# Performance work log

Measured on AMD Instinct MI355X. Metric: run time of the kernel, lower is better.

Reference implementation:

```python
import jax, jax.numpy as jnp
from jax import lax
import numpy as np

BLOCK = 256
EPS = 1e-6


def rms_norm(x, w):
    var = jnp.mean(jnp.square(x), axis=-1, keepdims=True)
    return x * lax.rsqrt(var + EPS) * w


def lightning_attn(q, k, v, slope):
    # q,k,v: [b,h,n,d]; slope: [h] positive decay rates
    b, h, n, d = q.shape
    nb = n // BLOCK
    ar = jnp.arange(1, BLOCK + 1, dtype=q.dtype)          # [BLOCK]
    s = slope[:, None, None]                               # [h,1,1]
    q_decay = jnp.exp(-s * ar[:, None])                    # [h,BLOCK,1]
    k_decay = jnp.exp(-s * (BLOCK - ar)[:, None])          # [h,BLOCK,1]
    idx = ar[:, None] - ar[None, :]                        # [BLOCK,BLOCK]
    diag_decay = jnp.exp(jnp.where(idx >= 0, -s * idx, -jnp.inf))  # [h,B,B]
    block_decay = jnp.exp(-slope * BLOCK)[None, :, None, None]     # [1,h,1,1]

    def to_blocks(x):
        return jnp.moveaxis(x.reshape(b, h, nb, BLOCK, d), 2, 0)   # [nb,b,h,B,d]

    qb, kb, vb = to_blocks(q), to_blocks(k), to_blocks(v)

    def step(kv, blk):
        qi, ki, vi = blk                                   # [b,h,B,d]
        inter = jnp.einsum('bhmd,bhde->bhme', qi * q_decay, kv)
        qk = jnp.einsum('bhmd,bhkd->bhmk', qi, ki) * diag_decay
        intra = jnp.einsum('bhmk,bhke->bhme', qk, vi)
        kv_new = block_decay * kv + jnp.einsum('bhmd,bhme->bhde', ki * k_decay, vi)
        return kv_new, inter + intra

    kv0 = jnp.zeros((b, h, d, d), q.dtype)
    kv, out = lax.scan(step, kv0, (qb, kb, vb))            # out: [nb,b,h,B,d]
    out = jnp.moveaxis(out, 0, 2).reshape(b, h, n, d)
    return out, kv


def setup_inputs() -> dict:
    key = jax.random.key(0)
    ks = jax.random.split(key, 6)
    b, n, hidden, h, dh = 2, 4096, 2048, 16, 128
    return {
        'hidden_states': jax.random.normal(ks[0], (b, n, hidden), jnp.float32),
        'slope_rate': jax.random.uniform(ks[1], (h,), jnp.float32, 1e-3, 0.2),
        'w_qkv': jax.random.normal(ks[2], (3 * h * dh, hidden), jnp.float32) * 0.02,
        'w_gate': jax.random.normal(ks[3], (h * dh, hidden), jnp.float32) * 0.02,
        'w_out': jax.random.normal(ks[4], (hidden, h * dh), jnp.float32) * 0.02,
        'norm_w': jnp.ones((h * dh,), jnp.float32),
    }


def reference(hidden_states, slope_rate, w_qkv, w_gate, w_out, norm_w):
    b, n, hidden = hidden_states.shape
    h = slope_rate.shape[0]
    dh = hidden // h
    qkv = jax.nn.silu(hidden_states @ w_qkv.T)             # [b,n,3*h*dh]
    qkv = qkv.reshape(b, n, 3, h, dh)
    q = jnp.transpose(qkv[:, :, 0], (0, 2, 1, 3))          # [b,h,n,dh]
    k = jnp.transpose(qkv[:, :, 1], (0, 2, 1, 3))
    v = jnp.transpose(qkv[:, :, 2], (0, 2, 1, 3))
    attn_out, _kv = lightning_attn(q, k, v, slope_rate)
    attn_out = jnp.transpose(attn_out, (0, 2, 1, 3)).reshape(b, n, h * dh)
    out = rms_norm(attn_out, norm_w)
    gate = jax.nn.sigmoid(hidden_states @ w_gate.T)
    out = (gate * out) @ w_out.T
    return out
```

## Files before the change

### kernel.cpp

```cpp
#include <hip/hip_runtime.h>


typedef unsigned short u16;
typedef __bf16 bf16x8 __attribute__((ext_vector_type(8)));
typedef float f32x4 __attribute__((ext_vector_type(4)));

#define SEQ 4096
#define HID 2048

__device__ __forceinline__ u16 f2bf(float f) {
    union { float f; unsigned u; } v; v.f = f;
    unsigned r = v.u + 0x7fffu + ((v.u >> 16) & 1u);
    return (u16)(r >> 16);
}
__device__ __forceinline__ float bf2f(u16 u) {
    union { unsigned u; float f; } v; v.u = ((unsigned)u) << 16; return v.f;
}

typedef __attribute__((address_space(1))) unsigned char gas_u8;
typedef __attribute__((address_space(3))) unsigned char las_u8;
__device__ __forceinline__ void gld16(const void* g, void* l) {
    __builtin_amdgcn_global_load_lds((gas_u8*)g, (las_u8*)l, 16, 0, 0);
}

__global__ __launch_bounds__(256) void castk(const float* __restrict__ in,
                                             u16* __restrict__ out) {
    const size_t i = (size_t)blockIdx.x * 256 + threadIdx.x;
    const float4 f = *(const float4*)&in[i * 4];
    uint2 o;
    o.x = (unsigned)f2bf(f.x) | ((unsigned)f2bf(f.y) << 16);
    o.y = (unsigned)f2bf(f.z) | ((unsigned)f2bf(f.w) << 16);
    *(uint2*)&out[i * 4] = o;
}

template <int MODE>
__global__ __launch_bounds__(512, 2) void gemm256(const u16* __restrict__ A,
                                                  const u16* __restrict__ Bm,
                                                  void* __restrict__ Cv,
                                                  void* __restrict__ aux,
                                                  void* __restrict__ aux2) {
    constexpr int NTN = (MODE == 0) ? 32 : 8;
    constexpr int NT  = 32;
    extern __shared__ u16 smem[];

    const int bid = blockIdx.x;
    const int xcd = bid & 7, l = bid >> 3;
    int tm, tn;
    if constexpr (MODE == 0) {
        tm = xcd * 4 + (l & 3);
        tn = ((l >> 2) & 7) | ((l >> 5) << 3);
    } else {
        const int wgid = xcd * 32 + l;
        tm = wgid / NTN; tn = wgid % NTN;
    }

    const int tid  = threadIdx.x;
    const int lane = tid & 63, wv = tid >> 6;
    const int quad = lane >> 4, cl = lane & 15;
    const int wm = (wv & 1) * 128, wn = (wv >> 1) * 64;

    const int srw  = tid >> 3;
    const int colo = ((tid & 7) ^ (srw & 7)) * 8;
    const u16* gA0 = A  + (size_t)(tm * 256 + srw) * HID + colo;
    const u16* gB0 = Bm + (size_t)(tn * 256 + srw) * HID + colo;

    const int x0 = ((quad       ^ (cl & 7)) * 8);
    const int x1 = (((4 + quad) ^ (cl & 7)) * 8);

    f32x4 acc[8][4];
    const f32x4 zero = {0.f, 0.f, 0.f, 0.f};
    #pragma unroll
    for (int a = 0; a < 8; a++)
        #pragma unroll
        for (int b = 0; b < 4; b++) acc[a][b] = zero;

    bf16x8 af[8], b0[4], b1[4];

    auto STG = [&](int kt, int mat, int hh) {
        const u16* g = (mat ? gB0 : gA0) + (size_t)(hh * 128) * HID + kt * 64;
        u16* lp = smem + (kt & 1) * 32768 + mat * 16384 + hh * 8192 + wv * 512;
        gld16(g, lp);
        gld16(g + (size_t)64 * HID, lp + 4096);
    };
    auto LDA = [&](int qm, int ab) {
        #pragma unroll
        for (int mi = 0; mi < 4; mi++) {
            const int rr = (wm + qm * 64 + mi * 16 + cl) * 64 + ab;
            af[mi * 2 + 0] = *(const bf16x8*)&smem[rr + x0];
            af[mi * 2 + 1] = *(const bf16x8*)&smem[rr + x1];
        }
    };
    auto LDB = [&](bf16x8* d, int qn, int bb2) {
        #pragma unroll
        for (int ni = 0; ni < 2; ni++) {
            const int rr = (wn + qn * 32 + ni * 16 + cl) * 64 + bb2;
            d[ni * 2 + 0] = *(const bf16x8*)&smem[rr + x0];
            d[ni * 2 + 1] = *(const bf16x8*)&smem[rr + x1];
        }
    };
    auto MM = [&](int qm, int qn, const bf16x8* bv) {
        #pragma unroll
        for (int mi = 0; mi < 4; mi++)
            #pragma unroll
            for (int ni = 0; ni < 2; ni++) {
                f32x4 c = acc[qm * 4 + mi][qn * 2 + ni];
                c = __builtin_amdgcn_mfma_f32_16x16x32_bf16(af[mi * 2 + 0], bv[ni * 2 + 0], c, 0, 0, 0);
                c = __builtin_amdgcn_mfma_f32_16x16x32_bf16(af[mi * 2 + 1], bv[ni * 2 + 1], c, 0, 0, 0);
                acc[qm * 4 + mi][qn * 2 + ni] = c;
            }
    };

    STG(0, 1, 0); STG(0, 1, 1); STG(0, 0, 0); STG(0, 0, 1);
    STG(1, 1, 0); STG(1, 1, 1); STG(1, 0, 0);
    asm volatile("s_waitcnt vmcnt(6)" ::: "memory");
    __builtin_amdgcn_s_barrier();
    LDA(0, 0); LDB(b0, 0, 16384);

    #pragma unroll 2
    for (int t = 0; t < NT; ++t) {
        const int ab  = (t & 1) * 32768;
        const int bb2 = ab + 16384;
        const int nab = ((t + 1) & 1) * 32768;
        if (t + 1 < NT) STG(t + 1, 0, 1);
        __builtin_amdgcn_s_barrier();
        asm volatile("s_waitcnt lgkmcnt(0)" ::: "memory");
        __builtin_amdgcn_s_setprio(1); MM(0, 0, b0); __builtin_amdgcn_s_setprio(0);
        LDB(b1, 1, bb2);
        __builtin_amdgcn_s_barrier();
        if (t + 2 < NT) STG(t + 2, 1, 0);
        __builtin_amdgcn_s_barrier();
        asm volatile("s_waitcnt lgkmcnt(0)" ::: "memory");
        __builtin_amdgcn_s_setprio(1); MM(0, 1, b1); __builtin_amdgcn_s_setprio(0);
        LDA(1, ab);
        __builtin_amdgcn_s_barrier();
        if (t + 2 < NT) STG(t + 2, 1, 1);
        __builtin_amdgcn_s_barrier();
        asm volatile("s_waitcnt lgkmcnt(0)" ::: "memory");
        __builtin_amdgcn_s_setprio(1); MM(1, 1, b1); __builtin_amdgcn_s_setprio(0);
        __builtin_amdgcn_s_barrier();
        if (t + 2 < NT) {
            STG(t + 2, 0, 0);
            asm volatile("s_waitcnt vmcnt(6)" ::: "memory");
        } else {
            asm volatile("s_waitcnt vmcnt(0)" ::: "memory");
        }
        __builtin_amdgcn_s_barrier();
        __builtin_amdgcn_s_setprio(1); MM(1, 0, b0); __builtin_amdgcn_s_setprio(0);
        if (t + 1 < NT) { LDA(0, nab); LDB(b0, 0, nab + 16384); }
        __builtin_amdgcn_s_barrier();
    }

    if constexpr (MODE == 0) {
        const int grp = tn * 2 + (wn >> 7);
        const int which = grp >> 4, hd = grp & 15;
        const int n64 = wn & 64;
        if (which == 2) {
            const size_t bz = (size_t)((tm >> 4) * 256 + hd * 16 + (tm & 15));
            u16* tdst = (u16*)aux + bz * 32768;
            #pragma unroll
            for (int a = 0; a < 8; a++) {
                const int mm = wm + (a >> 2) * 64 + (a & 3) * 16 + quad * 4;
                #pragma unroll
                for (int b = 0; b < 4; b++) {
                    const int d = n64 + (b >> 1) * 32 + (b & 1) * 16 + cl;
                    u16 p[4];
                    #pragma unroll
                    for (int r = 0; r < 4; r++) {
                        const float x = acc[a][b][r];
                        p[r] = f2bf(x / (1.f + __expf(-x)));
                    }
                    uint2 pk;
                    pk.x = (unsigned)p[0] | ((unsigned)p[1] << 16);
                    pk.y = (unsigned)p[2] | ((unsigned)p[3] << 16);
                    *(uint2*)&tdst[(size_t)d * 256 + mm] = pk;
                }
            }
            return;
        }
        u16* dst = (which == 0) ? (u16*)Cv
                 : (which == 1) ? (u16*)Cv + (size_t)16777216
                                : (u16*)aux2;
        #pragma unroll
        for (int a = 0; a < 8; a++)
            #pragma unroll
            for (int b = 0; b < 4; b++)
                #pragma unroll
                for (int r = 0; r < 4; r++) {
                    const int m = tm * 256 + wm + (a >> 2) * 64 + (a & 3) * 16 + quad * 4 + r;
                    const int col = hd * 128 + n64 + (b >> 1) * 32 + (b & 1) * 16 + cl;
                    const float x = acc[a][b][r];
                    const float v = (which == 3) ? 1.f / (1.f + __expf(-x))
                                                 : x / (1.f + __expf(-x));
                    dst[(size_t)m * HID + col] = f2bf(v);
                }
        return;
    } else {
        float* C = (float*)Cv;
        #pragma unroll
        for (int a = 0; a < 8; a++)
            #pragma unroll
            for (int b = 0; b < 4; b++)
                #pragma unroll
                for (int r = 0; r < 4; r++) {
                    const int m = tm * 256 + wm + (a >> 2) * 64 + (a & 3) * 16 + quad * 4 + r;
                    const int n = tn * 256 + wn + (b >> 1) * 32 + (b & 1) * 16 + cl;
                    C[(size_t)m * HID + n] = acc[a][b][r];
                }
    }
}

#define M_KVT   4

template <int MODE>
__global__ __launch_bounds__(256) void gemm_nt(const u16* __restrict__ A,
                                               const u16* __restrict__ Bm,
                                               void* __restrict__ Cv,
                                               const float* __restrict__ slope,
                                               int bz0,
                                               void* __restrict__ aux,
                                               void* __restrict__ aux2) {
    const int tid = threadIdx.x;
    const int bz  = blockIdx.z + bz0;

    __shared__ u16 smem[8192];
    u16 (*As)[32] = (u16(*)[32])smem;
    u16 (*Bs)[32] = (u16(*)[32])(smem + 4096);

    const int lane = tid & 63, wv = tid >> 6;
    const int wm = (wv & 1) * 64, wn = (wv >> 1) * 64;
    const int quad = lane >> 4, cl = lane & 15;
    const int lr = lane >> 2;
    const int lc = (lane & 3) * 8;
    u16* lA = &As[wv * 32][0];
    u16* lB = &Bs[wv * 32][0];

    f32x4 acc[4][4];
    const f32x4 zero = {0.f, 0.f, 0.f, 0.f};
    #pragma unroll
    for (int mi = 0; mi < 4; mi++)
        #pragma unroll
        for (int ni = 0; ni < 4; ni++) acc[mi][ni] = zero;

    const u16* Ab = A + (size_t)bz * 32768;
    const u16* Bb = Bm + (size_t)bz * 32768;
    const u16* gA = Ab + (size_t)(wv * 32 + lr) * 256 + lc;
    const u16* gB = Bb + (size_t)(wv * 32 + lr) * 256 + lc;

    for (int k0 = 0; k0 < 256; k0 += 32) {
        __syncthreads();
        gld16(gA + k0,                  lA);
        gld16(gA + k0 + (size_t)16 * 256, lA + 16 * 32);
        gld16(gB + k0,                  lB);
        gld16(gB + k0 + (size_t)16 * 256, lB + 16 * 32);
        __syncthreads();
        const int ko = quad * 8;
        bf16x8 af[4], bfv[4];
        #pragma unroll
        for (int mi = 0; mi < 4; mi++) af[mi] = *(const bf16x8*)&As[wm + mi * 16 + cl][ko];
        #pragma unroll
        for (int ni = 0; ni < 4; ni++) bfv[ni] = *(const bf16x8*)&Bs[wn + ni * 16 + cl][ko];
        #pragma unroll
        for (int mi = 0; mi < 4; mi++)
            #pragma unroll
            for (int ni = 0; ni < 4; ni++)
                acc[mi][ni] = __builtin_amdgcn_mfma_f32_16x16x32_bf16(af[mi], bfv[ni], acc[mi][ni], 0, 0, 0);
    }

    #pragma unroll
    for (int mi = 0; mi < 4; mi++)
        #pragma unroll
        for (int ni = 0; ni < 4; ni++)
            #pragma unroll
            for (int r = 0; r < 4; r++) {
                const int m = wm + mi * 16 + quad * 4 + r;
                const int n = wn + ni * 16 + cl;
                ((float*)Cv)[(size_t)bz * 16384 + m * 128 + n] = acc[mi][ni][r];
            }
}

__global__ __launch_bounds__(256) void fused_pv(const u16* __restrict__ qb,
                                                const u16* __restrict__ kb,
                                                const u16* __restrict__ ST,
                                                const u16* __restrict__ vT,
                                                u16* __restrict__ attn,
                                                const float* __restrict__ slope) {
    __shared__ u16 smem[28672];
    u16* q_lds = smem;
    u16* k_lds = smem + 16384;
    u16* P_lds = smem + 20480;
    u16* Bs    = smem + 24576;

    const int tm = blockIdx.x;
    const int bz = blockIdx.z;
    const int bb = bz >> 8, hh = (bz >> 4) & 15, jb = bz & 15;
    const float s_ = slope[hh];

    const int tid  = threadIdx.x;
    const int lane = tid & 63, wv = tid >> 6;
    const int quad = lane >> 4, cl = lane & 15;
    const int wm = (wv & 1) * 64, wn = (wv >> 1) * 64;
    const int lr = lane >> 2, lc = (lane & 3) * 8;
    const int pcb = (wv >> 1) * 16;

    const size_t rowbase = (size_t)(bb * SEQ + jb * 256);

    const u16* gq = qb + (rowbase + tm * 128 + wv * 32 + lr) * HID + hh * 128 + lc;
    u16* lq = q_lds + wv * 1024 + lr * 32 + lc;
    #pragma unroll
    for (int ks = 0; ks < 4; ks++) {
        gld16(gq + ks * 32,                 lq + ks * 4096);
        gld16(gq + ks * 32 + 16 * HID,      lq + ks * 4096 + 512);
    }

    f32x4 acc[4][4];
    const f32x4 zero = {0.f, 0.f, 0.f, 0.f};
    #pragma unroll
    for (int mi = 0; mi < 4; mi++)
        #pragma unroll
        for (int ni = 0; ni < 4; ni++) acc[mi][ni] = zero;

    const u16* gS = ST + (size_t)bz * 16384 + (size_t)(wv * 32 + lr) * 128 + lc;
    u16* lB = Bs + wv * 1024 + lr * 32 + lc;
    #pragma unroll
    for (int ks = 0; ks < 4; ks++) {
        __syncthreads();
        gld16(gS + ks * 32,            lB);
        gld16(gS + ks * 32 + 16 * 128, lB + 512);
        __syncthreads();
        bf16x8 af[4], bfv[4];
        #pragma unroll
        for (int mi = 0; mi < 4; mi++)
            af[mi] = *(const bf16x8*)&q_lds[ks * 4096 + (wm + mi * 16 + cl) * 32 + quad * 8];
        #pragma unroll
        for (int ni = 0; ni < 4; ni++)
            bfv[ni] = *(const bf16x8*)&Bs[(wn + ni * 16 + cl) * 32 + quad * 8];
        #pragma unroll
        for (int mi = 0; mi < 4; mi++)
            #pragma unroll
            for (int ni = 0; ni < 4; ni++)
                acc[mi][ni] = __builtin_amdgcn_mfma_f32_16x16x32_bf16(af[mi], bfv[ni], acc[mi][ni], 0, 0, 0);
    }
    #pragma unroll
    for (int mi = 0; mi < 4; mi++)
        #pragma unroll
        for (int r = 0; r < 4; r++) {
            const int m = tm * 128 + wm + mi * 16 + quad * 4 + r;
            const float qd = __expf(-s_ * (float)(m + 1));
            #pragma unroll
            for (int ni = 0; ni < 4; ni++) acc[mi][ni][r] *= qd;
        }

    const int kmax = (tm == 0) ? 128 : 256;
    const u16* gV = vT + (size_t)bz * 32768 + (size_t)(wv * 32 + lr) * 256 + lc;
    const int krow = tid >> 4;
    const int kcol = (((tid & 15) ^ (krow & 7)) * 8);
    u16* lk = k_lds + wv * 512 + lane * 8;
    const int kvr = pcb + cl;

    for (int kv0 = 0; kv0 < kmax; kv0 += 32) {
        __syncthreads();
        gld16(kb + (rowbase + kv0 +      krow) * HID + hh * 128 + kcol, lk);
        gld16(kb + (rowbase + kv0 + 16 + krow) * HID + hh * 128 + kcol, lk + 2048);
        gld16(gV + kv0,            lB);
        gld16(gV + kv0 + 16 * 256, lB + 512);
        __syncthreads();
        f32x4 acc2[4];
        #pragma unroll
        for (int mi = 0; mi < 4; mi++) acc2[mi] = zero;
        #pragma unroll
        for (int ds = 0; ds < 4; ds++) {
            bf16x8 bk = *(const bf16x8*)&k_lds[kvr * 128 + (((ds * 4 + quad) ^ (kvr & 7)) * 8)];
            #pragma unroll
            for (int mi = 0; mi < 4; mi++) {
                bf16x8 aq = *(const bf16x8*)&q_lds[ds * 4096 + (wm + mi * 16 + cl) * 32 + quad * 8];
                acc2[mi] = __builtin_amdgcn_mfma_f32_16x16x32_bf16(aq, bk, acc2[mi], 0, 0, 0);
            }
        }
        #pragma unroll
        for (int mi = 0; mi < 4; mi++)
            #pragma unroll
            for (int r = 0; r < 4; r++) {
                const int row = wm + mi * 16 + quad * 4 + r;
                const int mb  = tm * 128 + row;
                const int kv  = kv0 + pcb + cl;
                const int d   = mb - kv;
                const float x = acc2[mi][r];
                P_lds[row * 32 + pcb + cl] = f2bf(d >= 0 ? x * __expf(-s_ * (float)d) : 0.f);
            }
        __syncthreads();
        bf16x8 afp[4], bfv[4];
        #pragma unroll
        for (int mi = 0; mi < 4; mi++)
            afp[mi] = *(const bf16x8*)&P_lds[(wm + mi * 16 + cl) * 32 + quad * 8];
        #pragma unroll
        for (int ni = 0; ni < 4; ni++)
            bfv[ni] = *(const bf16x8*)&Bs[(wn + ni * 16 + cl) * 32 + quad * 8];
        #pragma unroll
        for (int mi = 0; mi < 4; mi++)
            #pragma unroll
            for (int ni = 0; ni < 4; ni++)
                acc[mi][ni] = __builtin_amdgcn_mfma_f32_16x16x32_bf16(afp[mi], bfv[ni], acc[mi][ni], 0, 0, 0);
    }

    #pragma unroll
    for (int mi = 0; mi < 4; mi++)
        #pragma unroll
        for (int ni = 0; ni < 4; ni++)
            #pragma unroll
            for (int r = 0; r < 4; r++) {
                const int m = tm * 128 + wm + mi * 16 + quad * 4 + r;
                const int n = wn + ni * 16 + cl;
                attn[(rowbase + m) * HID + hh * 128 + n] = f2bf(acc[mi][ni][r]);
            }
}

__global__ __launch_bounds__(256) void transpose_k(const u16* __restrict__ kb,
                                                   u16* __restrict__ kTs,
                                                   const float* __restrict__ slope) {
    __shared__ u16 t[128][137];
    const int bz = blockIdx.x;
    const int bb = bz >> 8, hh = (bz >> 4) & 15, jb = bz & 15;
    const int tid = threadIdx.x;
    const float s_ = slope[hh];
    const u16* src = kb + ((size_t)(bb * SEQ + jb * 256)) * HID + hh * 128;
    u16* dst = kTs + (size_t)bz * 32768;

    for (int half = 0; half < 2; half++) {
        #pragma unroll
        for (int i = 0; i < 8; i++) {
            const int flat = tid + 256 * i;
            const int row = flat >> 4, c8 = (flat & 15) * 8;
            *(uint4*)&t[row][c8] = *(const uint4*)&src[(size_t)(half * 128 + row) * HID + c8];
        }
        __syncthreads();
        #pragma unroll
        for (int i = 0; i < 8; i++) {
            const int flat = tid + 256 * i;
            const int d = flat >> 4, mc = (flat & 15) * 8;
            u16 p[8];
            #pragma unroll
            for (int j = 0; j < 8; j++) {
                const int m = half * 128 + mc + j;
                p[j] = f2bf(bf2f(t[mc + j][d]) * __expf(-s_ * (float)(255 - m)));
            }
            uint4 pk;
            pk.x = (unsigned)p[0] | ((unsigned)p[1] << 16);
            pk.y = (unsigned)p[2] | ((unsigned)p[3] << 16);
            pk.z = (unsigned)p[4] | ((unsigned)p[5] << 16);
            pk.w = (unsigned)p[6] | ((unsigned)p[7] << 16);
            *(uint4*)&dst[(size_t)d * 256 + half * 128 + mc] = pk;
        }
        __syncthreads();
    }
}

__global__ __launch_bounds__(256) void scan_kv(const float* __restrict__ KVT,
                                               u16* __restrict__ ST,
                                               const float* __restrict__ slope) {
    const int bh = blockIdx.x >> 4, ch = blockIdx.x & 15;
    const int off = ch * 1024 + threadIdx.x * 4;
    const float bd = __expf(-256.f * slope[bh & 15]);
    float4 st = {0.f, 0.f, 0.f, 0.f};
    for (int j = 0; j < 16; j++) {
        const size_t base = ((size_t)(bh * 16 + j)) * 16384 + off;
        uint2 o;
        o.x = (unsigned)f2bf(st.x) | ((unsigned)f2bf(st.y) << 16);
        o.y = (unsigned)f2bf(st.z) | ((unsigned)f2bf(st.w) << 16);
        *(uint2*)&ST[base] = o;
        const float4 kv = *(const float4*)&KVT[base];
        st.x = bd * st.x + kv.x;
        st.y = bd * st.y + kv.y;
        st.z = bd * st.z + kv.z;
        st.w = bd * st.w + kv.w;
    }
}

__global__ __launch_bounds__(256) void rmsnorm_gate(const u16* __restrict__ attn,
                                                    const u16* __restrict__ gate,
                                                    const float* __restrict__ nw,
                                                    u16* __restrict__ y) {
    const int r = blockIdx.x, tid = threadIdx.x;
    const size_t base = (size_t)r * HID + tid * 8;
    const uint4 a = *(const uint4*)&attn[base];
    float x[8];
    x[0] = bf2f(a.x & 0xffff); x[1] = bf2f(a.x >> 16);
    x[2] = bf2f(a.y & 0xffff); x[3] = bf2f(a.y >> 16);
    x[4] = bf2f(a.z & 0xffff); x[5] = bf2f(a.z >> 16);
    x[6] = bf2f(a.w & 0xffff); x[7] = bf2f(a.w >> 16);
    float s = 0.f;
    #pragma unroll
    for (int i = 0; i < 8; i++) s += x[i] * x[i];
    #pragma unroll
    for (int off = 32; off > 0; off >>= 1) s += __shfl_down(s, off);
    __shared__ float red[4];
    if ((tid & 63) == 0) red[tid >> 6] = s;
    __syncthreads();
    const float tot = red[0] + red[1] + red[2] + red[3];
    const float sc = rsqrtf(tot * (1.f / 2048.f) + 1e-6f);
    const uint4 g = *(const uint4*)&gate[base];
    float gv[8];
    gv[0] = bf2f(g.x & 0xffff); gv[1] = bf2f(g.x >> 16);
    gv[2] = bf2f(g.y & 0xffff); gv[3] = bf2f(g.y >> 16);
    gv[4] = bf2f(g.z & 0xffff); gv[5] = bf2f(g.z >> 16);
    gv[6] = bf2f(g.w & 0xffff); gv[7] = bf2f(g.w >> 16);
    const float4 w0 = *(const float4*)&nw[tid * 8];
    const float4 w1 = *(const float4*)&nw[tid * 8 + 4];
    const float wv[8] = {w0.x, w0.y, w0.z, w0.w, w1.x, w1.y, w1.z, w1.w};
    u16 o[8];
    #pragma unroll
    for (int i = 0; i < 8; i++) o[i] = f2bf(gv[i] * x[i] * sc * wv[i]);
    uint4 ov;
    ov.x = (unsigned)o[0] | ((unsigned)o[1] << 16);
    ov.y = (unsigned)o[2] | ((unsigned)o[3] << 16);
    ov.z = (unsigned)o[4] | ((unsigned)o[5] << 16);
    ov.w = (unsigned)o[6] | ((unsigned)o[7] << 16);
    *(uint4*)&y[base] = ov;
}

extern "C" void kernel_launch(void* const* d_in, const int* in_sizes, int n_in,
                              void* d_out, int out_size, void* d_ws, size_t ws_size,
                              hipStream_t stream) {
    const float* hidden = (const float*)d_in[0];
    const float* slope  = (const float*)d_in[1];
    const float* w_qkv  = (const float*)d_in[2];
    const float* w_gate = (const float*)d_in[3];
    const float* w_out  = (const float*)d_in[4];
    const float* norm_w = (const float*)d_in[5];
    float* out = (float*)d_out;

    char* w = (char*)d_ws;
    u16* qb   = (u16*)(w);
    u16* kb   = (u16*)(w +  33554432);
    u16* kTs  = (u16*)(w +  67108864);
    u16* hid_bf = (u16*)(w + 100663296);
    u16* vT   = (u16*)(w + 134217728);
    u16* gate = (u16*)(w + 167772160);
    u16* wqkv_bf  = (u16*)(w + 201326592);
    u16* wgate_bf = (u16*)(w + 201326592 + 25165824);
    float* KVT  = (float*)hid_bf;
    u16*   ST   = kTs;
    u16*   wout_bf = kb;
    u16*   attn = wqkv_bf;
    u16*   y    = kTs;

    static bool s_attr = false;
    if (!s_attr) {
        (void)hipFuncSetAttribute((const void*)gemm256<0>,
                                  hipFuncAttributeMaxDynamicSharedMemorySize, 131072);
        (void)hipFuncSetAttribute((const void*)gemm256<1>,
                                  hipFuncAttributeMaxDynamicSharedMemorySize, 131072);
        s_attr = true;
    }

    castk<<<16384, 256, 0, stream>>>(hidden, hid_bf);
    castk<<<12288, 256, 0, stream>>>(w_qkv,  wqkv_bf);
    castk<<< 4096, 256, 0, stream>>>(w_gate, wgate_bf);

    gemm256<0><<<dim3(1024), dim3(512), 131072, stream>>>(hid_bf, wqkv_bf, qb, vT, gate);
    transpose_k     <<<512,             256, 0, stream>>>(kb, kTs, slope);
    gemm_nt<M_KVT ><<<dim3(1, 1, 512),  256, 0, stream>>>(vT, kTs, KVT, slope, 0, nullptr, nullptr);
    scan_kv         <<<512,             256, 0, stream>>>(KVT, ST, slope);
    fused_pv        <<<dim3(2, 1, 512), 256, 0, stream>>>(qb, kb, ST, vT, attn, slope);
    castk<<< 4096, 256, 0, stream>>>(w_out, wout_bf);
    rmsnorm_gate    <<<8192,            256, 0, stream>>>(attn, gate, norm_w, y);
    gemm256<1><<<dim3(256), dim3(512), 131072, stream>>>(y, wout_bf, (void*)out, nullptr, nullptr);
}
```

Before: 447.9 us.

## Fuse K transpose-decay into QKV GEMM epilogue and merge cast kernels

The QKV GEMM epilogue now writes the decayed, transposed K tile directly into the kTs buffer, so the separate transpose_k kernel and its re-read of K from global memory are gone. The three fp32-to-bf16 cast launches are merged into one kernel that picks its source by block range. In exchange the GEMM epilogue does extra exp work, and the transposed stores are 8-byte writes strided across rows, which may coalesce poorly and add register pressure to the epilogue.

```diff
diff --git a/kernel.cpp b/kernel.cpp
--- a/kernel.cpp
+++ b/kernel.cpp
@@ -33,12 +33,29 @@
     *(uint2*)&out[i * 4] = o;
 }
 
+__global__ __launch_bounds__(256) void castk3(const float* __restrict__ a, u16* __restrict__ ao,
+                                              const float* __restrict__ b, u16* __restrict__ bo,
+                                              const float* __restrict__ c, u16* __restrict__ co) {
+    const int bid = blockIdx.x;
+    const float* src; u16* dst; size_t i;
+    if (bid < 16384)      { src = a; dst = ao; i = (size_t)bid * 256 + threadIdx.x; }
+    else if (bid < 28672) { src = b; dst = bo; i = (size_t)(bid - 16384) * 256 + threadIdx.x; }
+    else                  { src = c; dst = co; i = (size_t)(bid - 28672) * 256 + threadIdx.x; }
+    const float4 f = *(const float4*)&src[i * 4];
+    uint2 o;
+    o.x = (unsigned)f2bf(f.x) | ((unsigned)f2bf(f.y) << 16);
+    o.y = (unsigned)f2bf(f.z) | ((unsigned)f2bf(f.w) << 16);
+    *(uint2*)&dst[i * 4] = o;
+}
+
 template <int MODE>
 __global__ __launch_bounds__(512, 2) void gemm256(const u16* __restrict__ A,
                                                   const u16* __restrict__ Bm,
                                                   void* __restrict__ Cv,
                                                   void* __restrict__ aux,
-                                                  void* __restrict__ aux2) {
+                                                  void* __restrict__ aux2,
+                                                  u16* __restrict__ kTs,
+                                                  const float* __restrict__ slope) {
     constexpr int NTN = (MODE == 0) ? 32 : 8;
     constexpr int NT  = 32;
     extern __shared__ u16 smem[];
@@ -193,6 +210,30 @@
                                                  : x / (1.f + __expf(-x));
                     dst[(size_t)m * HID + col] = f2bf(v);
                 }
+        if (which == 1) {
+            const float s_ = slope[hd];
+            const size_t bz = (size_t)((tm >> 4) * 256 + hd * 16 + (tm & 15));
+            u16* tdst = kTs + bz * 32768;
+            #pragma unroll
+            for (int a = 0; a < 8; a++) {
+                const int mm = wm + (a >> 2) * 64 + (a & 3) * 16 + quad * 4;
+                #pragma unroll
+                for (int b = 0; b < 4; b++) {
+                    const int d = n64 + (b >> 1) * 32 + (b & 1) * 16 + cl;
+                    u16 p[4];
+                    #pragma unroll
+                    for (int r = 0; r < 4; r++) {
+                        const float x = acc[a][b][r];
+                        const float sv = x / (1.f + __expf(-x));
+                        p[r] = f2bf(sv * __expf(-s_ * (float)(255 - (mm + r))));
+                    }
+                    uint2 pk;
+                    pk.x = (unsigned)p[0] | ((unsigned)p[1] << 16);
+                    pk.y = (unsigned)p[2] | ((unsigned)p[3] << 16);
+                    *(uint2*)&tdst[(size_t)d * 256 + mm] = pk;
+                }
+            }
+        }
         return;
     } else {
         float* C = (float*)Cv;
@@ -412,46 +453,6 @@
                 const int n = wn + ni * 16 + cl;
                 attn[(rowbase + m) * HID + hh * 128 + n] = f2bf(acc[mi][ni][r]);
             }
-}
-
-__global__ __launch_bounds__(256) void transpose_k(const u16* __restrict__ kb,
-                                                   u16* __restrict__ kTs,
-                                                   const float* __restrict__ slope) {
-    __shared__ u16 t[128][137];
-    const int bz = blockIdx.x;
-    const int bb = bz >> 8, hh = (bz >> 4) & 15, jb = bz & 15;
-    const int tid = threadIdx.x;
-    const float s_ = slope[hh];
-    const u16* src = kb + ((size_t)(bb * SEQ + jb * 256)) * HID + hh * 128;
-    u16* dst = kTs + (size_t)bz * 32768;
-
-    for (int half = 0; half < 2; half++) {
-        #pragma unroll
-        for (int i = 0; i < 8; i++) {
-            const int flat = tid + 256 * i;
-            const int row = flat >> 4, c8 = (flat & 15) * 8;
-            *(uint4*)&t[row][c8] = *(const uint4*)&src[(size_t)(half * 128 + row) * HID + c8];
-        }
-        __syncthreads();
-        #pragma unroll
-        for (int i = 0; i < 8; i++) {
-            const int flat = tid + 256 * i;
-            const int d = flat >> 4, mc = (flat & 15) * 8;
-            u16 p[8];
-            #pragma unroll
-            for (int j = 0; j < 8; j++) {
-                const int m = half * 128 + mc + j;
-                p[j] = f2bf(bf2f(t[mc + j][d]) * __expf(-s_ * (float)(255 - m)));
-            }
-            uint4 pk;
-            pk.x = (unsigned)p[0] | ((unsigned)p[1] << 16);
-            pk.y = (unsigned)p[2] | ((unsigned)p[3] << 16);
-            pk.z = (unsigned)p[4] | ((unsigned)p[5] << 16);
-            pk.w = (unsigned)p[6] | ((unsigned)p[7] << 16);
-            *(uint4*)&dst[(size_t)d * 256 + half * 128 + mc] = pk;
-        }
-        __syncthreads();
-    }
 }
 
 __global__ __launch_bounds__(256) void scan_kv(const float* __restrict__ KVT,
@@ -552,16 +553,13 @@
         s_attr = true;
     }
 
-    castk<<<16384, 256, 0, stream>>>(hidden, hid_bf);
-    castk<<<12288, 256, 0, stream>>>(w_qkv,  wqkv_bf);
-    castk<<< 4096, 256, 0, stream>>>(w_gate, wgate_bf);
-
-    gemm256<0><<<dim3(1024), dim3(512), 131072, stream>>>(hid_bf, wqkv_bf, qb, vT, gate);
-    transpose_k     <<<512,             256, 0, stream>>>(kb, kTs, slope);
+    castk3<<<32768, 256, 0, stream>>>(hidden, hid_bf, w_qkv, wqkv_bf, w_gate, wgate_bf);
+
+    gemm256<0><<<dim3(1024), dim3(512), 131072, stream>>>(hid_bf, wqkv_bf, qb, vT, gate, kTs, slope);
     gemm_nt<M_KVT ><<<dim3(1, 1, 512),  256, 0, stream>>>(vT, kTs, KVT, slope, 0, nullptr, nullptr);
     scan_kv         <<<512,             256, 0, stream>>>(KVT, ST, slope);
     fused_pv        <<<dim3(2, 1, 512), 256, 0, stream>>>(qb, kb, ST, vT, attn, slope);
     castk<<< 4096, 256, 0, stream>>>(w_out, wout_bf);
     rmsnorm_gate    <<<8192,            256, 0, stream>>>(attn, gate, norm_w, y);
-    gemm256<1><<<dim3(256), dim3(512), 131072, stream>>>(y, wout_bf, (void*)out, nullptr, nullptr);
-}
+    gemm256<1><<<dim3(256), dim3(512), 131072, stream>>>(y, wout_bf, (void*)out, nullptr, nullptr, nullptr, nullptr);
+}
```

New measurement: 448.7 us. Within noise of the previous version (+0.2%).

## Double-buffer K/V chunk loads in fused_pv and merge input casts into one kernel

Applied to the files above, without the earlier changes.

The fused_pv inner loop now double-buffers the K and V chunks in LDS. It issues the next chunk's async global-to-LDS loads before computing on the current one, and replaces __syncthreads with explicit vmcnt/lgkmcnt waits plus raw barriers. This is meant to hide global load latency behind the QK^T and PV MFMAs. LDS per block rises from 56 to 72 KB, which may lower occupancy, and the hand-written waitcnt logic is easy to get wrong. Separately, the three fp32-to-bf16 cast launches are merged into one kernel to save launch overhead.

```diff
diff --git a/kernel.cpp b/kernel.cpp
--- a/kernel.cpp
+++ b/kernel.cpp
@@ -31,6 +31,21 @@
     o.x = (unsigned)f2bf(f.x) | ((unsigned)f2bf(f.y) << 16);
     o.y = (unsigned)f2bf(f.z) | ((unsigned)f2bf(f.w) << 16);
     *(uint2*)&out[i * 4] = o;
+}
+
+__global__ __launch_bounds__(256) void castk3(const float* __restrict__ a, u16* __restrict__ ao,
+                                              const float* __restrict__ b, u16* __restrict__ bo,
+                                              const float* __restrict__ c, u16* __restrict__ co) {
+    const int bid = blockIdx.x;
+    const float* src; u16* dst; size_t i;
+    if (bid < 16384)      { src = a; dst = ao; i = (size_t)bid * 256 + threadIdx.x; }
+    else if (bid < 28672) { src = b; dst = bo; i = (size_t)(bid - 16384) * 256 + threadIdx.x; }
+    else                  { src = c; dst = co; i = (size_t)(bid - 28672) * 256 + threadIdx.x; }
+    const float4 f = *(const float4*)&src[i * 4];
+    uint2 o;
+    o.x = (unsigned)f2bf(f.x) | ((unsigned)f2bf(f.y) << 16);
+    o.y = (unsigned)f2bf(f.z) | ((unsigned)f2bf(f.w) << 16);
+    *(uint2*)&dst[i * 4] = o;
 }
 
 template <int MODE>
@@ -284,11 +299,11 @@
                                                 const u16* __restrict__ vT,
                                                 u16* __restrict__ attn,
                                                 const float* __restrict__ slope) {
-    __shared__ u16 smem[28672];
+    __shared__ u16 smem[36864];
     u16* q_lds = smem;
     u16* k_lds = smem + 16384;
-    u16* P_lds = smem + 20480;
-    u16* Bs    = smem + 24576;
+    u16* P_lds = smem + 24576;
+    u16* Bs    = smem + 28672;
 
     const int tm = blockIdx.x;
     const int bz = blockIdx.z;
@@ -349,33 +364,48 @@
             #pragma unroll
             for (int ni = 0; ni < 4; ni++) acc[mi][ni][r] *= qd;
         }
+    __syncthreads();
 
     const int kmax = (tm == 0) ? 128 : 256;
+    const int nc   = kmax >> 5;
     const u16* gV = vT + (size_t)bz * 32768 + (size_t)(wv * 32 + lr) * 256 + lc;
     const int krow = tid >> 4;
     const int kcol = (((tid & 15) ^ (krow & 7)) * 8);
-    u16* lk = k_lds + wv * 512 + lane * 8;
     const int kvr = pcb + cl;
 
-    for (int kv0 = 0; kv0 < kmax; kv0 += 32) {
-        __syncthreads();
+    auto stage_chunk = [&](int c, int buf) {
+        u16* lk = k_lds + buf * 4096 + wv * 512 + lane * 8;
+        u16* lv = Bs + buf * 4096 + wv * 1024 + lr * 32 + lc;
+        const int kv0 = c * 32;
         gld16(kb + (rowbase + kv0 +      krow) * HID + hh * 128 + kcol, lk);
         gld16(kb + (rowbase + kv0 + 16 + krow) * HID + hh * 128 + kcol, lk + 2048);
-        gld16(gV + kv0,            lB);
-        gld16(gV + kv0 + 16 * 256, lB + 512);
-        __syncthreads();
+        gld16(gV + kv0,            lv);
+        gld16(gV + kv0 + 16 * 256, lv + 512);
+    };
+
+    stage_chunk(0, 0);
+    for (int c = 0; c < nc; ++c) {
+        const int cb = c & 1;
+        if (c + 1 < nc) {
+            stage_chunk(c + 1, cb ^ 1);
+            asm volatile("s_waitcnt vmcnt(4)" ::: "memory");
+        } else {
+            asm volatile("s_waitcnt vmcnt(0)" ::: "memory");
+        }
+        __builtin_amdgcn_s_barrier();
         f32x4 acc2[4];
         #pragma unroll
         for (int mi = 0; mi < 4; mi++) acc2[mi] = zero;
         #pragma unroll
         for (int ds = 0; ds < 4; ds++) {
-            bf16x8 bk = *(const bf16x8*)&k_lds[kvr * 128 + (((ds * 4 + quad) ^ (kvr & 7)) * 8)];
+            bf16x8 bk = *(const bf16x8*)&k_lds[cb * 4096 + kvr * 128 + (((ds * 4 + quad) ^ (kvr & 7)) * 8)];
             #pragma unroll
             for (int mi = 0; mi < 4; mi++) {
                 bf16x8 aq = *(const bf16x8*)&q_lds[ds * 4096 + (wm + mi * 16 + cl) * 32 + quad * 8];
                 acc2[mi] = __builtin_amdgcn_mfma_f32_16x16x32_bf16(aq, bk, acc2[mi], 0, 0, 0);
             }
         }
+        const int kv0 = c * 32;
         #pragma unroll
         for (int mi = 0; mi < 4; mi++)
             #pragma unroll
@@ -387,19 +417,21 @@
                 const float x = acc2[mi][r];
                 P_lds[row * 32 + pcb + cl] = f2bf(d >= 0 ? x * __expf(-s_ * (float)d) : 0.f);
             }
-        __syncthreads();
+        asm volatile("s_waitcnt lgkmcnt(0)" ::: "memory");
+        __builtin_amdgcn_s_barrier();
         bf16x8 afp[4], bfv[4];
         #pragma unroll
         for (int mi = 0; mi < 4; mi++)
             afp[mi] = *(const bf16x8*)&P_lds[(wm + mi * 16 + cl) * 32 + quad * 8];
         #pragma unroll
         for (int ni = 0; ni < 4; ni++)
-            bfv[ni] = *(const bf16x8*)&Bs[(wn + ni * 16 + cl) * 32 + quad * 8];
+            bfv[ni] = *(const bf16x8*)&Bs[cb * 4096 + (wn + ni * 16 + cl) * 32 + quad * 8];
         #pragma unroll
         for (int mi = 0; mi < 4; mi++)
             #pragma unroll
             for (int ni = 0; ni < 4; ni++)
                 acc[mi][ni] = __builtin_amdgcn_mfma_f32_16x16x32_bf16(afp[mi], bfv[ni], acc[mi][ni], 0, 0, 0);
+        __builtin_amdgcn_s_barrier();
     }
 
     #pragma unroll
@@ -552,9 +584,7 @@
         s_attr = true;
     }
 
-    castk<<<16384, 256, 0, stream>>>(hidden, hid_bf);
-    castk<<<12288, 256, 0, stream>>>(w_qkv,  wqkv_bf);
-    castk<<< 4096, 256, 0, stream>>>(w_gate, wgate_bf);
+    castk3<<<32768, 256, 0, stream>>>(hidden, hid_bf, w_qkv, wqkv_bf, w_gate, wgate_bf);
 
     gemm256<0><<<dim3(1024), dim3(512), 131072, stream>>>(hid_bf, wqkv_bf, qb, vT, gate);
     transpose_k     <<<512,             256, 0, stream>>>(kb, kTs, slope);
```

New measurement: 443.4 us. Within noise of the previous version (-1.0%).
